# Kernel tuning notes

Measured on AMD Instinct MI355X. Metric: run time of the kernel, lower is better.

## Reference

```python
import jax, jax.numpy as jnp
import numpy as np

ALPHA = 0.1
STEPS = 4


def setup_inputs() -> dict:
    key = jax.random.key(0)
    x = jax.random.normal(key, (4, 8192, 1024), dtype=jnp.float32)
    return {"x": x}


def reference(x) -> jnp.ndarray:
    # CtaPostAttnMixer.forward, layout='bld', prefill, steps=4, alpha=0.1
    # Fixed-boundary 1D heat-diffusion stencil along the sequence dim.
    if x.shape[1] < 3:
        return x
    y = x.astype(jnp.float32)
    for _ in range(STEPS):
        # Laplacian on interior tokens: y[l+1] - 2 y[l] + y[l-1]
        lap = y[:, 2:, :] - 2.0 * y[:, 1:-1, :] + y[:, :-2, :]
        y = jnp.concatenate(
            [y[:, :1, :], y[:, 1:-1, :] + ALPHA * lap, y[:, -1:, :]], axis=1
        )
    return y.astype(x.dtype)
```

## Files before the change

kernel.cpp:

```cpp
#include <hip/hip_runtime.h>


namespace {

constexpr int Lr   = 8192;
constexpr int Dq   = 1024 / 4;
constexpr int Bn   = 4;
constexpr int C    = 4;
constexpr int W    = C + 8;
constexpr int SEGS = Lr / C;
constexpr int NXCD = 8;
constexpr int NWG  = SEGS * Bn;

constexpr float WK0 = 0.4870f;
constexpr float WK1 = 0.2144f;
constexpr float WK2 = 0.0388f;
constexpr float WK3 = 0.0032f;
constexpr float WK4 = 0.0001f;

typedef float nfloat4 __attribute__((ext_vector_type(4)));

__device__ __forceinline__ float4 f4_add(float4 a, float4 b) {
    return make_float4(a.x + b.x, a.y + b.y, a.z + b.z, a.w + b.w);
}
__device__ __forceinline__ float4 f4_mul(float s, float4 a) {
    return make_float4(s * a.x, s * a.y, s * a.z, s * a.w);
}
__device__ __forceinline__ float4 f4_fma(float s, float4 a, float4 c) {
    return make_float4(fmaf(s, a.x, c.x), fmaf(s, a.y, c.y),
                       fmaf(s, a.z, c.z), fmaf(s, a.w, c.w));
}
__device__ __forceinline__ void f4_store_nt(float4* p, float4 v) {
    nfloat4 nv;
    nv.x = v.x; nv.y = v.y; nv.z = v.z; nv.w = v.w;
    __builtin_nontemporal_store(nv, (nfloat4*)p);
}

__global__ __launch_bounds__(256, 8)
void mixer4_kernel(const float4* __restrict__ x, float4* __restrict__ y) {
    const int d4  = threadIdx.x;

    const int lin = blockIdx.x;
    const int g   = (lin & (NXCD - 1)) * (NWG / NXCD) + (lin >> 3);
    const int b   = g >> 11;
    const int seg = g & (SEGS - 1);

    const int c0  = seg * C;

    const float4* __restrict__ xb = x + (size_t)b * Lr * Dq + d4;
    float4* __restrict__       yb = y + (size_t)b * Lr * Dq + d4;

    float4 w[W];
#pragma unroll
    for (int i = 0; i < W; ++i) {
        int gl = c0 - 4 + i;
        gl = gl < 0 ? 0 : gl;
        gl = gl > Lr - 1 ? Lr - 1 : gl;
        w[i] = xb[(size_t)gl * Dq];
    }

    if (c0 != 0 && c0 != Lr - C) {
#pragma unroll
        for (int j = 0; j < C; ++j) {
            float4 acc = f4_mul(WK0, w[j + 4]);
            acc = f4_fma(WK1, f4_add(w[j + 3], w[j + 5]), acc);
            acc = f4_fma(WK2, f4_add(w[j + 2], w[j + 6]), acc);
            acc = f4_fma(WK3, f4_add(w[j + 1], w[j + 7]), acc);
            acc = f4_fma(WK4, f4_add(w[j + 0], w[j + 8]), acc);
            f4_store_nt(&yb[(size_t)(c0 + j) * Dq], acc);
        }
    } else if (c0 == 0) {
        f4_store_nt(&yb[0], w[4]);
        {
            float4 o = f4_mul(0.2986f, w[4]);
            o = f4_fma(0.4482f, w[5], o);
            o = f4_fma(0.2112f, w[6], o);
            o = f4_fma(0.0387f, w[7], o);
            o = f4_fma(0.0032f, w[8], o);
            o = f4_fma(0.0001f, w[9], o);
            f4_store_nt(&yb[(size_t)1 * Dq], o);
        }
        {
            float4 o = f4_mul(0.0454f, w[4]);
            o = f4_fma(0.2112f, w[5], o);
            o = f4_fma(0.4869f, w[6], o);
            o = f4_fma(0.2144f, w[7], o);
            o = f4_fma(0.0388f, w[8], o);
            o = f4_fma(0.0032f, w[9], o);
            o = f4_fma(0.0001f, w[10], o);
            f4_store_nt(&yb[(size_t)2 * Dq], o);
        }
        {
            float4 o = f4_mul(0.0034f, w[4]);
            o = f4_fma(0.0387f, w[5], o);
            o = f4_fma(0.2144f, w[6], o);
            o = f4_fma(0.4870f, w[7], o);
            o = f4_fma(0.2144f, w[8], o);
            o = f4_fma(0.0388f, w[9], o);
            o = f4_fma(0.0032f, w[10], o);
            o = f4_fma(0.0001f, w[11], o);
            f4_store_nt(&yb[(size_t)3 * Dq], o);
        }
    } else {
        f4_store_nt(&yb[(size_t)(Lr - 1) * Dq], w[7]);
        {
            float4 o = f4_mul(0.2986f, w[7]);
            o = f4_fma(0.4482f, w[6], o);
            o = f4_fma(0.2112f, w[5], o);
            o = f4_fma(0.0387f, w[4], o);
            o = f4_fma(0.0032f, w[3], o);
            o = f4_fma(0.0001f, w[2], o);
            f4_store_nt(&yb[(size_t)(Lr - 2) * Dq], o);
        }
        {
            float4 o = f4_mul(0.0454f, w[7]);
            o = f4_fma(0.2112f, w[6], o);
            o = f4_fma(0.4869f, w[5], o);
            o = f4_fma(0.2144f, w[4], o);
            o = f4_fma(0.0388f, w[3], o);
            o = f4_fma(0.0032f, w[2], o);
            o = f4_fma(0.0001f, w[1], o);
            f4_store_nt(&yb[(size_t)(Lr - 3) * Dq], o);
        }
        {
            float4 o = f4_mul(0.0034f, w[7]);
            o = f4_fma(0.0387f, w[6], o);
            o = f4_fma(0.2144f, w[5], o);
            o = f4_fma(0.4870f, w[4], o);
            o = f4_fma(0.2144f, w[3], o);
            o = f4_fma(0.0388f, w[2], o);
            o = f4_fma(0.0032f, w[1], o);
            o = f4_fma(0.0001f, w[0], o);
            f4_store_nt(&yb[(size_t)(Lr - 4) * Dq], o);
        }
    }
}

}

extern "C" void kernel_launch(void* const* d_in, const int* in_sizes, int n_in,
                              void* d_out, int out_size, void* d_ws, size_t ws_size,
                              hipStream_t stream) {
    const float4* x = (const float4*)d_in[0];
    float4*       y = (float4*)d_out;

    dim3 grid(NWG);
    dim3 block(256);
    hipLaunchKernelGGL(mixer4_kernel, grid, block, 0, stream, x, y);
}
```

Before: 236.2 us.

## Process 16 rows per workgroup with rolling register window to cut halo reloads

Each workgroup now covers 16 sequence rows instead of 4, streaming the input through a rotating three-buffer register window of four rows each and computing the 9-tap stencil in four phases. Per-workgroup halo overhead drops from 8 extra rows per 4 outputs to 8 per 16, which reduces redundant global loads and cuts the grid size by a factor of four. Loads for the next phase are issued before the current phase's compute so memory latency can overlap. Register pressure rises, so occupancy hint is lowered from 8 to 6.

```diff
diff --git a/kernel.cpp b/kernel.cpp
--- a/kernel.cpp
+++ b/kernel.cpp
@@ -6,8 +6,7 @@
 constexpr int Lr   = 8192;
 constexpr int Dq   = 1024 / 4;
 constexpr int Bn   = 4;
-constexpr int C    = 4;
-constexpr int W    = C + 8;
+constexpr int C    = 16;
 constexpr int SEGS = Lr / C;
 constexpr int NXCD = 8;
 constexpr int NWG  = SEGS * Bn;
@@ -36,103 +35,140 @@
     __builtin_nontemporal_store(nv, (nfloat4*)p);
 }
 
-__global__ __launch_bounds__(256, 8)
+__device__ __forceinline__ void interior_phase(
+        float4* __restrict__ yb, int r0,
+        const float4 (&P)[4], const float4 (&Q)[4], const float4 (&R)[4]) {
+    float4 w[12];
+#pragma unroll
+    for (int i = 0; i < 4; ++i) { w[i] = P[i]; w[i + 4] = Q[i]; w[i + 8] = R[i]; }
+#pragma unroll
+    for (int j = 0; j < 4; ++j) {
+        float4 acc = f4_mul(WK0, w[j + 4]);
+        acc = f4_fma(WK1, f4_add(w[j + 3], w[j + 5]), acc);
+        acc = f4_fma(WK2, f4_add(w[j + 2], w[j + 6]), acc);
+        acc = f4_fma(WK3, f4_add(w[j + 1], w[j + 7]), acc);
+        acc = f4_fma(WK4, f4_add(w[j + 0], w[j + 8]), acc);
+        f4_store_nt(&yb[(size_t)(r0 + j) * Dq], acc);
+    }
+}
+
+__device__ __forceinline__ void boundary_low(
+        float4* __restrict__ yb, const float4 (&Q)[4], const float4 (&R)[4]) {
+    f4_store_nt(&yb[0], Q[0]);
+    {
+        float4 o = f4_mul(0.2986f, Q[0]);
+        o = f4_fma(0.4482f, Q[1], o);
+        o = f4_fma(0.2112f, Q[2], o);
+        o = f4_fma(0.0387f, Q[3], o);
+        o = f4_fma(0.0032f, R[0], o);
+        o = f4_fma(0.0001f, R[1], o);
+        f4_store_nt(&yb[(size_t)1 * Dq], o);
+    }
+    {
+        float4 o = f4_mul(0.0454f, Q[0]);
+        o = f4_fma(0.2112f, Q[1], o);
+        o = f4_fma(0.4869f, Q[2], o);
+        o = f4_fma(0.2144f, Q[3], o);
+        o = f4_fma(0.0388f, R[0], o);
+        o = f4_fma(0.0032f, R[1], o);
+        o = f4_fma(0.0001f, R[2], o);
+        f4_store_nt(&yb[(size_t)2 * Dq], o);
+    }
+    {
+        float4 o = f4_mul(0.0034f, Q[0]);
+        o = f4_fma(0.0387f, Q[1], o);
+        o = f4_fma(0.2144f, Q[2], o);
+        o = f4_fma(0.4870f, Q[3], o);
+        o = f4_fma(0.2144f, R[0], o);
+        o = f4_fma(0.0388f, R[1], o);
+        o = f4_fma(0.0032f, R[2], o);
+        o = f4_fma(0.0001f, R[3], o);
+        f4_store_nt(&yb[(size_t)3 * Dq], o);
+    }
+}
+
+__device__ __forceinline__ void boundary_high(
+        float4* __restrict__ yb, const float4 (&P)[4], const float4 (&Q)[4]) {
+    f4_store_nt(&yb[(size_t)(Lr - 1) * Dq], Q[3]);
+    {
+        float4 o = f4_mul(0.2986f, Q[3]);
+        o = f4_fma(0.4482f, Q[2], o);
+        o = f4_fma(0.2112f, Q[1], o);
+        o = f4_fma(0.0387f, Q[0], o);
+        o = f4_fma(0.0032f, P[3], o);
+        o = f4_fma(0.0001f, P[2], o);
+        f4_store_nt(&yb[(size_t)(Lr - 2) * Dq], o);
+    }
+    {
+        float4 o = f4_mul(0.0454f, Q[3]);
+        o = f4_fma(0.2112f, Q[2], o);
+        o = f4_fma(0.4869f, Q[1], o);
+        o = f4_fma(0.2144f, Q[0], o);
+        o = f4_fma(0.0388f, P[3], o);
+        o = f4_fma(0.0032f, P[2], o);
+        o = f4_fma(0.0001f, P[1], o);
+        f4_store_nt(&yb[(size_t)(Lr - 3) * Dq], o);
+    }
+    {
+        float4 o = f4_mul(0.0034f, Q[3]);
+        o = f4_fma(0.0387f, Q[2], o);
+        o = f4_fma(0.2144f, Q[1], o);
+        o = f4_fma(0.4870f, Q[0], o);
+        o = f4_fma(0.2144f, P[3], o);
+        o = f4_fma(0.0388f, P[2], o);
+        o = f4_fma(0.0032f, P[1], o);
+        o = f4_fma(0.0001f, P[0], o);
+        f4_store_nt(&yb[(size_t)(Lr - 4) * Dq], o);
+    }
+}
+
+__global__ __launch_bounds__(256, 6)
 void mixer4_kernel(const float4* __restrict__ x, float4* __restrict__ y) {
     const int d4  = threadIdx.x;
 
     const int lin = blockIdx.x;
     const int g   = (lin & (NXCD - 1)) * (NWG / NXCD) + (lin >> 3);
-    const int b   = g >> 11;
+    const int b   = g >> 9;
     const int seg = g & (SEGS - 1);
-
     const int c0  = seg * C;
 
     const float4* __restrict__ xb = x + (size_t)b * Lr * Dq + d4;
     float4* __restrict__       yb = y + (size_t)b * Lr * Dq + d4;
 
-    float4 w[W];
+    auto ld = [&](int row) -> float4 {
+        row = row < 0 ? 0 : row;
+        row = row > Lr - 1 ? Lr - 1 : row;
+        return xb[(size_t)row * Dq];
+    };
+
+    float4 A[4], B[4], Cb[4];
 #pragma unroll
-    for (int i = 0; i < W; ++i) {
-        int gl = c0 - 4 + i;
-        gl = gl < 0 ? 0 : gl;
-        gl = gl > Lr - 1 ? Lr - 1 : gl;
-        w[i] = xb[(size_t)gl * Dq];
+    for (int i = 0; i < 4; ++i) A[i]  = ld(c0 - 4 + i);
+#pragma unroll
+    for (int i = 0; i < 4; ++i) B[i]  = ld(c0 + i);
+#pragma unroll
+    for (int i = 0; i < 4; ++i) Cb[i] = ld(c0 + 4 + i);
+
+    if (seg != 0) {
+        interior_phase(yb, c0, A, B, Cb);
+    } else {
+        boundary_low(yb, B, Cb);
     }
+#pragma unroll
+    for (int i = 0; i < 4; ++i) A[i] = ld(c0 + 8 + i);
 
-    if (c0 != 0 && c0 != Lr - C) {
+    interior_phase(yb, c0 + 4, B, Cb, A);
 #pragma unroll
-        for (int j = 0; j < C; ++j) {
-            float4 acc = f4_mul(WK0, w[j + 4]);
-            acc = f4_fma(WK1, f4_add(w[j + 3], w[j + 5]), acc);
-            acc = f4_fma(WK2, f4_add(w[j + 2], w[j + 6]), acc);
-            acc = f4_fma(WK3, f4_add(w[j + 1], w[j + 7]), acc);
-            acc = f4_fma(WK4, f4_add(w[j + 0], w[j + 8]), acc);
-            f4_store_nt(&yb[(size_t)(c0 + j) * Dq], acc);
-        }
-    } else if (c0 == 0) {
-        f4_store_nt(&yb[0], w[4]);
-        {
-            float4 o = f4_mul(0.2986f, w[4]);
-            o = f4_fma(0.4482f, w[5], o);
-            o = f4_fma(0.2112f, w[6], o);
-            o = f4_fma(0.0387f, w[7], o);
-            o = f4_fma(0.0032f, w[8], o);
-            o = f4_fma(0.0001f, w[9], o);
-            f4_store_nt(&yb[(size_t)1 * Dq], o);
-        }
-        {
-            float4 o = f4_mul(0.0454f, w[4]);
-            o = f4_fma(0.2112f, w[5], o);
-            o = f4_fma(0.4869f, w[6], o);
-            o = f4_fma(0.2144f, w[7], o);
-            o = f4_fma(0.0388f, w[8], o);
-            o = f4_fma(0.0032f, w[9], o);
-            o = f4_fma(0.0001f, w[10], o);
-            f4_store_nt(&yb[(size_t)2 * Dq], o);
-        }
-        {
-            float4 o = f4_mul(0.0034f, w[4]);
-            o = f4_fma(0.0387f, w[5], o);
-            o = f4_fma(0.2144f, w[6], o);
-            o = f4_fma(0.4870f, w[7], o);
-            o = f4_fma(0.2144f, w[8], o);
-            o = f4_fma(0.0388f, w[9], o);
-            o = f4_fma(0.0032f, w[10], o);
-            o = f4_fma(0.0001f, w[11], o);
-            f4_store_nt(&yb[(size_t)3 * Dq], o);
-        }
+    for (int i = 0; i < 4; ++i) B[i] = ld(c0 + 12 + i);
+
+    interior_phase(yb, c0 + 8, Cb, A, B);
+#pragma unroll
+    for (int i = 0; i < 4; ++i) Cb[i] = ld(c0 + 16 + i);
+
+    if (seg != SEGS - 1) {
+        interior_phase(yb, c0 + 12, A, B, Cb);
     } else {
-        f4_store_nt(&yb[(size_t)(Lr - 1) * Dq], w[7]);
-        {
-            float4 o = f4_mul(0.2986f, w[7]);
-            o = f4_fma(0.4482f, w[6], o);
-            o = f4_fma(0.2112f, w[5], o);
-            o = f4_fma(0.0387f, w[4], o);
-            o = f4_fma(0.0032f, w[3], o);
-            o = f4_fma(0.0001f, w[2], o);
-            f4_store_nt(&yb[(size_t)(Lr - 2) * Dq], o);
-        }
-        {
-            float4 o = f4_mul(0.0454f, w[7]);
-            o = f4_fma(0.2112f, w[6], o);
-            o = f4_fma(0.4869f, w[5], o);
-            o = f4_fma(0.2144f, w[4], o);
-            o = f4_fma(0.0388f, w[3], o);
-            o = f4_fma(0.0032f, w[2], o);
-            o = f4_fma(0.0001f, w[1], o);
-            f4_store_nt(&yb[(size_t)(Lr - 3) * Dq], o);
-        }
-        {
-            float4 o = f4_mul(0.0034f, w[7]);
-            o = f4_fma(0.0387f, w[6], o);
-            o = f4_fma(0.2144f, w[5], o);
-            o = f4_fma(0.4870f, w[4], o);
-            o = f4_fma(0.2144f, w[3], o);
-            o = f4_fma(0.0388f, w[2], o);
-            o = f4_fma(0.0032f, w[1], o);
-            o = f4_fma(0.0001f, w[0], o);
-            f4_store_nt(&yb[(size_t)(Lr - 4) * Dq], o);
-        }
+        boundary_high(yb, A, B);
     }
 }
 
```

Result: slower. 242.7 us (+2.7%).
